# Performance work log

Measured on AMD Instinct MI355X. Metric: run time of the kernel, lower is better.

The kernel has to match this reference:

```python
import jax, jax.numpy as jnp
import numpy as np

B, N, D = 4, 2048, 512
H, DH = 8, 64
MLP = 2048
EPS = 1e-5


def setup_inputs() -> dict:
    key = jax.random.key(0)
    ks = jax.random.split(key, 8)
    s = lambda fan_in: 1.0 / np.sqrt(fan_in)
    return {
        "x": jax.random.normal(ks[0], (B, N, D), jnp.float32),
        "ln1_g": jnp.ones((D,), jnp.float32),
        "ln1_b": jnp.zeros((D,), jnp.float32),
        "Wqkv": jax.random.normal(ks[1], (D, 3 * H * DH), jnp.float32) * s(D),
        "temperature": jnp.asarray(np.log(DH ** -0.5), jnp.float32),
        "Wo": jax.random.normal(ks[2], (H * DH, D), jnp.float32) * s(H * DH),
        "bo": jnp.zeros((D,), jnp.float32),
        "ln2_g": jnp.ones((D,), jnp.float32),
        "ln2_b": jnp.zeros((D,), jnp.float32),
        "W1": jax.random.normal(ks[3], (D, MLP), jnp.float32) * s(D),
        "b1": jnp.zeros((MLP,), jnp.float32),
        "W2": jax.random.normal(ks[4], (MLP, D), jnp.float32) * s(MLP),
        "b2": jnp.zeros((D,), jnp.float32),
    }


def _layernorm(x, g, b):
    mu = jnp.mean(x, axis=-1, keepdims=True)
    var = jnp.var(x, axis=-1, keepdims=True)
    return (x - mu) * jax.lax.rsqrt(var + EPS) * g + b


def _lsa(x, Wqkv, temperature, Wo, bo):
    b, n, _ = x.shape
    qkv = x @ Wqkv  # [b, n, 3*H*DH]
    q, k, v = jnp.split(qkv, 3, axis=-1)
    rs = lambda t: t.reshape(b, n, H, DH).transpose(0, 2, 1, 3)  # b h n d
    q, k, v = rs(q), rs(k), rs(v)
    dots = jnp.einsum("bhnd,bhmd->bhnm", q, k) * jnp.exp(temperature)
    mask_value = -jnp.finfo(dots.dtype).max
    eye = jnp.eye(n, dtype=bool)
    dots = jnp.where(eye, mask_value, dots)  # mask diagonal (LSA)
    attn = jax.nn.softmax(dots, axis=-1)
    out = jnp.einsum("bhnm,bhmd->bhnd", attn, v)
    out = out.transpose(0, 2, 1, 3).reshape(b, n, H * DH)
    return out @ Wo + bo


def _ffn(x, W1, b1, W2, b2):
    h = jax.nn.gelu(x @ W1 + b1, approximate=False)
    return h @ W2 + b2


def reference(x, ln1_g, ln1_b, Wqkv, temperature, Wo, bo,
              ln2_g, ln2_b, W1, b1, W2, b2):
    y = _lsa(_layernorm(x, ln1_g, ln1_b), Wqkv, temperature, Wo, bo) + x
    z = _ffn(_layernorm(y, ln2_g, ln2_b), W1, b1, W2, b2) + y
    return (z, x)
```

## Files before the change

kernel.cpp:

```cpp
#include <hip/hip_runtime.h>
#include <math.h>

typedef __attribute__((ext_vector_type(4))) float f32x4;
typedef __attribute__((ext_vector_type(8))) short short8;

#define DEV __device__ __forceinline__

DEV short f2bf(float f){
  union { float f; unsigned u; } v; v.f = f;
  unsigned r = v.u + 0x7fffu + ((v.u >> 16) & 1u);
  return (short)(r >> 16);
}
DEV float bf2f(short s){
  union { unsigned u; float f; } v; v.u = ((unsigned)(unsigned short)s) << 16; return v.f;
}
DEV float exp2_hw(float x){ float r; asm("v_exp_f32 %0, %1" : "=v"(r) : "v"(x)); return r; }
DEV float rcp_hw(float x){ float r; asm("v_rcp_f32 %0, %1" : "=v"(r) : "v"(x)); return r; }
DEV unsigned cvtpk(float a, float b){
  unsigned r; asm("v_cvt_pk_bf16_f32 %0, %1, %2" : "=v"(r) : "v"(a), "v"(b)); return r;
}
DEV void gload_lds16(const short* src, short* lds){
  __builtin_amdgcn_global_load_lds(
      (const __attribute__((address_space(1))) void*)src,
      (__attribute__((address_space(3))) void*)lds, 16, 0, 0);
}
DEV float gelu_fast(float v){
  float u = v * (0.79788456f + 0.03567741f * v * v);
  float e = exp2_hw(u * 2.88539008f);
  float th = 1.0f - 2.0f * rcp_hw(e + 1.0f);
  return 0.5f * v * (1.0f + th);
}

__global__ __launch_bounds__(256) void transpose_bf16_kernel(
    const float* __restrict__ W, short* __restrict__ Wt, int K, int N)
{
  __shared__ float tile[32][33];
  int nb = blockIdx.x * 32, kb = blockIdx.y * 32;
  int tx = threadIdx.x & 31, ty = threadIdx.x >> 5;
  #pragma unroll
  for (int i = ty; i < 32; i += 8)
    tile[i][tx] = W[(size_t)(kb + i) * N + nb + tx];
  __syncthreads();
  #pragma unroll
  for (int i = ty; i < 32; i += 8)
    Wt[(size_t)(nb + i) * K + kb + tx] = f2bf(tile[tx][i]);
}

template<int COPYX>
__global__ __launch_bounds__(256) void ln_kernel(
    const float* __restrict__ x, const float* __restrict__ g,
    const float* __restrict__ b, short* __restrict__ out,
    float* __restrict__ xcopy)
{
  int row  = blockIdx.x * 4 + (threadIdx.x >> 6);
  int lane = threadIdx.x & 63;
  const float* xr = x + (size_t)row * 512 + lane * 8;
  f32x4 v0 = *(const f32x4*)(xr);
  f32x4 v1 = *(const f32x4*)(xr + 4);
  float s  = (v0[0]+v0[1]+v0[2]+v0[3]) + (v1[0]+v1[1]+v1[2]+v1[3]);
  float sq = (v0[0]*v0[0]+v0[1]*v0[1]+v0[2]*v0[2]+v0[3]*v0[3])
           + (v1[0]*v1[0]+v1[1]*v1[1]+v1[2]*v1[2]+v1[3]*v1[3]);
  #pragma unroll
  for (int off = 1; off < 64; off <<= 1) {
    s  += __shfl_xor(s, off);
    sq += __shfl_xor(sq, off);
  }
  float mu  = s * (1.0f / 512.0f);
  float var = sq * (1.0f / 512.0f) - mu * mu;
  float rstd = rsqrtf(var + 1e-5f);
  f32x4 g0 = *(const f32x4*)(g + lane * 8);
  f32x4 g1 = *(const f32x4*)(g + lane * 8 + 4);
  f32x4 b0 = *(const f32x4*)(b + lane * 8);
  f32x4 b1 = *(const f32x4*)(b + lane * 8 + 4);
  float o[8];
  #pragma unroll
  for (int j = 0; j < 4; ++j) o[j]     = (v0[j] - mu) * rstd * g0[j] + b0[j];
  #pragma unroll
  for (int j = 0; j < 4; ++j) o[4 + j] = (v1[j] - mu) * rstd * g1[j] + b1[j];
  uint4 pk;
  pk.x = cvtpk(o[0], o[1]); pk.y = cvtpk(o[2], o[3]);
  pk.z = cvtpk(o[4], o[5]); pk.w = cvtpk(o[6], o[7]);
  *(uint4*)(out + (size_t)row * 512 + lane * 8) = pk;
  if (COPYX) {
    float* xc = xcopy + (size_t)row * 512 + lane * 8;
    *(f32x4*)(xc)     = v0;
    *(f32x4*)(xc + 4) = v1;
  }
}

__global__ __launch_bounds__(256) void ln_bf_kernel(
    const short* __restrict__ x, const float* __restrict__ g,
    const float* __restrict__ b, short* __restrict__ out)
{
  int row  = blockIdx.x * 4 + (threadIdx.x >> 6);
  int lane = threadIdx.x & 63;
  short8 raw = *(const short8*)(x + (size_t)row * 512 + lane * 8);
  float v[8];
  #pragma unroll
  for (int j = 0; j < 8; ++j) v[j] = bf2f(raw[j]);
  float s = 0.f, sq = 0.f;
  #pragma unroll
  for (int j = 0; j < 8; ++j) { s += v[j]; sq += v[j] * v[j]; }
  #pragma unroll
  for (int off = 1; off < 64; off <<= 1) {
    s  += __shfl_xor(s, off);
    sq += __shfl_xor(sq, off);
  }
  float mu  = s * (1.0f / 512.0f);
  float var = sq * (1.0f / 512.0f) - mu * mu;
  float rstd = rsqrtf(var + 1e-5f);
  f32x4 g0 = *(const f32x4*)(g + lane * 8);
  f32x4 g1 = *(const f32x4*)(g + lane * 8 + 4);
  f32x4 b0 = *(const f32x4*)(b + lane * 8);
  f32x4 b1 = *(const f32x4*)(b + lane * 8 + 4);
  float o[8];
  #pragma unroll
  for (int j = 0; j < 4; ++j) o[j]     = (v[j] - mu) * rstd * g0[j] + b0[j];
  #pragma unroll
  for (int j = 0; j < 4; ++j) o[4 + j] = (v[4+j] - mu) * rstd * g1[j] + b1[j];
  uint4 pk;
  pk.x = cvtpk(o[0], o[1]); pk.y = cvtpk(o[2], o[3]);
  pk.z = cvtpk(o[4], o[5]); pk.w = cvtpk(o[6], o[7]);
  *(uint4*)(out + (size_t)row * 512 + lane * 8) = pk;
}

template<int EPI, int BM, typename OutT>
__global__ __launch_bounds__(256) void gemm_bt_kernel(
    const short* __restrict__ A, const short* __restrict__ Bt,
    OutT* __restrict__ C, const float* __restrict__ bias,
    const float* __restrict__ resid, const short* __restrict__ residb,
    int M, int N, int K)
{
  constexpr int MFR = BM / 32;
  constexpr int NFR = 4;
  constexpr int AI  = BM / 64;
  constexpr int BUF = BM * 32 + 128 * 32;
  __shared__ __align__(16) short smem[3 * BUF];

  int tid = threadIdx.x;
  int lane = tid & 63, wid = tid >> 6;
  int l16 = lane & 15, lq = lane >> 4;

  int gx = gridDim.x;
  int nwg = gx * gridDim.y;
  int orig = blockIdx.y * gx + blockIdx.x;
  int swz = (orig & 7) * (nwg >> 3) + (orig >> 3);
  int bn = swz % gx, bm = swz / gx;

  int wm = wid >> 1, wn = wid & 1;

  const short* gaP[AI];
  const short* gbP[2];
  #pragma unroll
  for (int i = 0; i < AI; ++i) {
    int gg = i * 4 + wid;
    gaP[i] = A + (size_t)(bm * BM + gg * 16 + l16) * K + lq * 8;
  }
  #pragma unroll
  for (int i = 0; i < 2; ++i) {
    int gg = i * 4 + wid;
    gbP[i] = Bt + (size_t)(bn * 128 + gg * 16 + l16) * K + lq * 8;
  }

  auto STAGE = [&](int bufi, int k0) {
    short* base = smem + bufi * BUF;
    #pragma unroll
    for (int i = 0; i < AI; ++i)
      gload_lds16(gaP[i] + k0, base + (i * 4 + wid) * 512);
    #pragma unroll
    for (int i = 0; i < 2; ++i)
      gload_lds16(gbP[i] + k0, base + BM * 32 + (i * 4 + wid) * 512);
  };

  f32x4 acc[MFR][NFR] = {};

  STAGE(0, 0);
  STAGE(1, 32);

  int nt = K >> 5;
  for (int t = 0; t < nt; ++t) {
    if (t + 1 < nt) {
      if constexpr (AI == 2) asm volatile("s_waitcnt vmcnt(4)" ::: "memory");
      else                   asm volatile("s_waitcnt vmcnt(3)" ::: "memory");
    } else {
      asm volatile("s_waitcnt vmcnt(0)" ::: "memory");
    }
    __builtin_amdgcn_s_barrier();
    __builtin_amdgcn_sched_barrier(0);
    if (t + 2 < nt) STAGE((t + 2) % 3, (t + 2) << 5);

    const short* base = smem + (t % 3) * BUF;
    short8 af[MFR], bfr[NFR];
    #pragma unroll
    for (int m = 0; m < MFR; ++m)
      af[m] = *(const short8*)(base + (wm * MFR + m) * 512 + lane * 8);
    #pragma unroll
    for (int n = 0; n < NFR; ++n)
      bfr[n] = *(const short8*)(base + BM * 32 + (wn * NFR + n) * 512 + lane * 8);
    __builtin_amdgcn_s_setprio(1);
    #pragma unroll
    for (int m = 0; m < MFR; ++m)
      #pragma unroll
      for (int n = 0; n < NFR; ++n)
        acc[m][n] = __builtin_amdgcn_mfma_f32_16x16x32_bf16(af[m], bfr[n], acc[m][n], 0, 0, 0);
    __builtin_amdgcn_s_setprio(0);
  }

  float bv[NFR];
  #pragma unroll
  for (int n = 0; n < NFR; ++n)
    bv[n] = bias[bn * 128 + (wn * NFR + n) * 16 + l16];

  #pragma unroll
  for (int m = 0; m < MFR; ++m) {
    #pragma unroll
    for (int r = 0; r < 4; ++r) {
      int row = bm * BM + (wm * MFR + m) * 16 + lq * 4 + r;
      #pragma unroll
      for (int n = 0; n < NFR; ++n) {
        int col = bn * 128 + (wn * NFR + n) * 16 + l16;
        float v = acc[m][n][r] + bv[n];
        if (EPI == 4) v += resid[(size_t)row * N + col];
        if (EPI == 5) v += bf2f(residb[(size_t)row * N + col]);
        if constexpr (sizeof(OutT) == 2)
          ((short*)C)[(size_t)row * N + col] = f2bf(v);
        else
          ((float*)C)[(size_t)row * N + col] = v;
      }
    }
  }
}

template<int EPI>
__global__ __launch_bounds__(512) void gemm256_kernel(
    const short* __restrict__ A, const short* __restrict__ Bt,
    short* __restrict__ C, const float* __restrict__ bias,
    short* __restrict__ vt, int M, int N, int K)
{
  constexpr int BUF = 24576;
  __shared__ __align__(16) short smem[3 * BUF];

  int tid = threadIdx.x;
  int lane = tid & 63, wid = tid >> 6;
  int l16 = lane & 15, lq = lane >> 4;

  int gx = gridDim.x;
  int nwg = gx * gridDim.y;
  int orig = blockIdx.y * gx + blockIdx.x;
  int swz = (orig & 7) * (nwg >> 3) + (orig >> 3);
  int bn = swz % gx, bm = swz / gx;

  int wm = wid >> 1, wn = wid & 1;

  const short* gaP[4];
  const short* gbP[2];
  #pragma unroll
  for (int i = 0; i < 4; ++i) {
    int g = i * 8 + wid;
    gaP[i] = A + (size_t)(bm * 256 + (g >> 1) * 16 + l16) * K + (g & 1) * 32 + lq * 8;
  }
  #pragma unroll
  for (int i = 0; i < 2; ++i) {
    int g = i * 8 + wid;
    gbP[i] = Bt + (size_t)(bn * 128 + (g >> 1) * 16 + l16) * K + (g & 1) * 32 + lq * 8;
  }

  auto STAGE = [&](int bufi, int k0) {
    short* base = smem + bufi * BUF;
    #pragma unroll
    for (int i = 0; i < 4; ++i)
      gload_lds16(gaP[i] + k0, base + (i * 8 + wid) * 512);
    #pragma unroll
    for (int i = 0; i < 2; ++i)
      gload_lds16(gbP[i] + k0, base + 16384 + (i * 8 + wid) * 512);
  };

  f32x4 acc[4][4] = {};

  STAGE(0, 0);
  STAGE(1, 64);

  int nt = K >> 6;
  for (int t = 0; t < nt; ++t) {
    if (t + 1 < nt) asm volatile("s_waitcnt vmcnt(6)" ::: "memory");
    else            asm volatile("s_waitcnt vmcnt(0)" ::: "memory");
    __builtin_amdgcn_s_barrier();
    __builtin_amdgcn_sched_barrier(0);
    if (t + 2 < nt) STAGE((t + 2) % 3, (t + 2) << 6);

    const short* base = smem + (t % 3) * BUF;
    #pragma unroll
    for (int kc = 0; kc < 2; ++kc) {
      short8 af[4], bfr[4];
      #pragma unroll
      for (int m = 0; m < 4; ++m)
        af[m] = *(const short8*)(base + ((wm * 4 + m) * 2 + kc) * 512 + lane * 8);
      #pragma unroll
      for (int n = 0; n < 4; ++n)
        bfr[n] = *(const short8*)(base + 16384 + ((wn * 4 + n) * 2 + kc) * 512 + lane * 8);
      __builtin_amdgcn_s_setprio(1);
      #pragma unroll
      for (int m = 0; m < 4; ++m)
        #pragma unroll
        for (int n = 0; n < 4; ++n)
          acc[m][n] = __builtin_amdgcn_mfma_f32_16x16x32_bf16(af[m], bfr[n], acc[m][n], 0, 0, 0);
      __builtin_amdgcn_s_setprio(0);
    }
  }

  if (EPI == 3 && bn >= 8) {
    __syncthreads();
    short* T = smem;
    #pragma unroll
    for (int m = 0; m < 4; ++m)
      #pragma unroll
      for (int n = 0; n < 4; ++n) {
        int c = wn * 64 + n * 16 + l16;
        #pragma unroll
        for (int r = 0; r < 4; ++r) {
          int rowl = wm * 64 + m * 16 + lq * 4 + r;
          T[c * 256 + (rowl ^ ((c & 7) << 4))] = f2bf(acc[m][n][r]);
        }
      }
    __syncthreads();
    int b2 = bm >> 3;
    int nnb = (bm & 7) * 256;
    int tn = tid & 31, cw = tid >> 5;
    #pragma unroll
    for (int c8 = 0; c8 < 8; ++c8) {
      int c = c8 * 16 + cw;
      short8 v = *(const short8*)(T + c * 256 + ((tn * 8) ^ ((c & 7) << 4)));
      if (tn & 1) {
        short8 w;
        #pragma unroll
        for (int j = 0; j < 8; ++j) w[j] = v[j ^ 4];
        v = w;
      }
      int c2 = bn * 128 + c - 1024;
      int bh = b2 * 8 + (c2 >> 6);
      int d  = c2 & 63;
      *(short8*)(vt + ((size_t)(bh * 64 + d)) * 2048 + nnb + tn * 8) = v;
    }
    return;
  }

  float bv[4];
  #pragma unroll
  for (int n = 0; n < 4; ++n)
    bv[n] = (EPI == 2) ? bias[bn * 128 + (wn * 4 + n) * 16 + l16] : 0.0f;

  #pragma unroll
  for (int m = 0; m < 4; ++m) {
    #pragma unroll
    for (int r = 0; r < 4; ++r) {
      int row = bm * 256 + (wm * 4 + m) * 16 + lq * 4 + r;
      #pragma unroll
      for (int n = 0; n < 4; ++n) {
        int col = bn * 128 + (wn * 4 + n) * 16 + l16;
        float v = acc[m][n][r];
        if (EPI == 2) v = gelu_fast(v + bv[n]);
        C[(size_t)row * N + col] = f2bf(v);
      }
    }
  }
}

__global__ __launch_bounds__(256, 2) void attn_kernel(
    const short* __restrict__ qkv, const short* __restrict__ vt,
    const float* __restrict__ temp_ptr,
    short* __restrict__ Op0, short* __restrict__ Op1, float* __restrict__ Lbuf)
{
  __shared__ __align__(16) short smem[16384];

  int tid = threadIdx.x;
  int lane = tid & 63, wid = tid >> 6;
  int l16 = lane & 15, lq = lane >> 4;
  int hi = lq >> 1, lq0 = lq & 1;

  int orig = blockIdx.y * 16 + blockIdx.x;
  int swz = (orig & 7) * 128 + (orig >> 3);
  int qb = swz & 15;
  int rr = swz >> 4;
  int bh = rr & 31, slice = rr >> 5;
  int b = bh >> 3, h = bh & 7;

  const short* qbase = qkv + (size_t)b * 2048 * 1536 + h * 64;
  const short* kbase = qbase + 512;
  const short* vbase = vt + (size_t)bh * 64 * 2048;
  int kslice = slice * 1024;

  float scale = __expf(temp_ptr[0]) * 1.44269504f;
  int q0 = qb * 128 + wid * 32;

  short8 qfrag[2][2];
  #pragma unroll
  for (int qf = 0; qf < 2; ++qf) {
    int qrow = q0 + qf * 16 + l16;
    #pragma unroll
    for (int c = 0; c < 2; ++c) {
      short8 raw = *(const short8*)(qbase + (size_t)qrow * 1536 + c * 32 + lq * 8);
      short8 sc;
      #pragma unroll
      for (int j = 0; j < 8; ++j) sc[j] = f2bf(bf2f(raw[j]) * scale);
      qfrag[qf][c] = sc;
    }
  }

  f32x4 accO[2][4] = {};
  float l[2] = {0.f, 0.f};

  auto STAGE = [&](int bufi, int k0) {
    #pragma unroll
    for (int i = 0; i < 2; ++i) {
      int w16 = i * 256 + tid;
      int sub = w16 >> 7;
      int cc  = (w16 >> 6) & 1;
      int lq2 = (w16 >> 4) & 3;
      int l2  = w16 & 15;
      const short* srcK = kbase + (size_t)(k0 + sub * 16 + l2) * 1536 + cc * 32 + lq2 * 8;
      gload_lds16(srcK, smem + bufi * 4096 + (i * 4 + wid) * 512);
      const short* srcV = vbase + (size_t)(sub * 16 + l2) * 2048 + k0 + cc * 32 + lq2 * 8;
      gload_lds16(srcV, smem + 8192 + bufi * 4096 + (i * 4 + wid) * 512);
    }
  };

  STAGE(0, kslice);
  asm volatile("s_waitcnt vmcnt(0)");
  __syncthreads();

  for (int t = 0; t < 16; ++t) {
    int cur = t & 1;
    int k0 = kslice + t * 64;
    if (t + 1 < 16) STAGE(cur ^ 1, k0 + 64);

    const short* kls = smem + cur * 4096;
    const short* vls = smem + 8192 + cur * 4096;

    f32x4 accS[2][4] = {};
    #pragma unroll
    for (int s = 0; s < 4; ++s) {
      short8 kf0 = *(const short8*)(kls + (s * 2 + 0) * 512 + lane * 8);
      short8 kf1 = *(const short8*)(kls + (s * 2 + 1) * 512 + lane * 8);
      #pragma unroll
      for (int qf = 0; qf < 2; ++qf) {
        accS[qf][s] = __builtin_amdgcn_mfma_f32_16x16x32_bf16(kf0, qfrag[qf][0], accS[qf][s], 0, 0, 0);
        accS[qf][s] = __builtin_amdgcn_mfma_f32_16x16x32_bf16(kf1, qfrag[qf][1], accS[qf][s], 0, 0, 0);
      }
    }

    if ((q0 & ~63) == k0) {
      #pragma unroll
      for (int qf = 0; qf < 2; ++qf) {
        int qg = q0 + qf * 16 + l16;
        #pragma unroll
        for (int s = 0; s < 4; ++s)
          #pragma unroll
          for (int r = 0; r < 4; ++r)
            if (k0 + s * 16 + lq * 4 + r == qg) accS[qf][s][r] = -30000.f;
      }
    }

    short8 pa[2][2];
    #pragma unroll
    for (int qf = 0; qf < 2; ++qf) {
      float sum = 0.f;
      unsigned W[4][2];
      #pragma unroll
      for (int s = 0; s < 4; ++s) {
        float p0 = exp2_hw(accS[qf][s][0]);
        float p1 = exp2_hw(accS[qf][s][1]);
        float p2 = exp2_hw(accS[qf][s][2]);
        float p3 = exp2_hw(accS[qf][s][3]);
        sum += (p0 + p1) + (p2 + p3);
        W[s][0] = cvtpk(p0, p1);
        W[s][1] = cvtpk(p2, p3);
      }
      sum += __shfl_xor(sum, 16);
      sum += __shfl_xor(sum, 32);
      l[qf] += sum;

      unsigned K0[2], S0[2], K2[2], S2[2], R0[2], R2[2];
      #pragma unroll
      for (int w = 0; w < 2; ++w) {
        K0[w] = hi ? W[1][w] : W[0][w];
        S0[w] = hi ? W[0][w] : W[1][w];
        K2[w] = hi ? W[3][w] : W[2][w];
        S2[w] = hi ? W[2][w] : W[3][w];
      }
      #pragma unroll
      for (int w = 0; w < 2; ++w) {
        R0[w] = (unsigned)__shfl_xor((int)S0[w], 32);
        R2[w] = (unsigned)__shfl_xor((int)S2[w], 32);
      }
      bool sw = (hi != lq0);
      unsigned FA[2], FB[2], sA[2], sB[2], GA[2], GB[2];
      #pragma unroll
      for (int w = 0; w < 2; ++w) {
        sA[w] = sw ? K0[w] : R0[w];  FA[w] = sw ? R0[w] : K0[w];
        sB[w] = sw ? K2[w] : R2[w];  FB[w] = sw ? R2[w] : K2[w];
      }
      #pragma unroll
      for (int w = 0; w < 2; ++w) {
        GA[w] = (unsigned)__shfl_xor((int)sA[w], 16);
        GB[w] = (unsigned)__shfl_xor((int)sB[w], 16);
      }
      union { unsigned u[4]; short8 s8; } p0u, p1u;
      p0u.u[0] = FA[0]; p0u.u[1] = FA[1]; p0u.u[2] = GA[0]; p0u.u[3] = GA[1];
      p1u.u[0] = FB[0]; p1u.u[1] = FB[1]; p1u.u[2] = GB[0]; p1u.u[3] = GB[1];
      pa[qf][0] = p0u.s8;
      pa[qf][1] = p1u.s8;
    }

    short8 vfr[4][2];
    #pragma unroll
    for (int d = 0; d < 4; ++d) {
      vfr[d][0] = *(const short8*)(vls + (d * 2 + 0) * 512 + lane * 8);
      vfr[d][1] = *(const short8*)(vls + (d * 2 + 1) * 512 + lane * 8);
    }
    #pragma unroll
    for (int qf = 0; qf < 2; ++qf)
      #pragma unroll
      for (int d = 0; d < 4; ++d) {
        accO[qf][d] = __builtin_amdgcn_mfma_f32_16x16x32_bf16(vfr[d][0], pa[qf][0], accO[qf][d], 0, 0, 0);
        accO[qf][d] = __builtin_amdgcn_mfma_f32_16x16x32_bf16(vfr[d][1], pa[qf][1], accO[qf][d], 0, 0, 0);
      }

    __syncthreads();
  }

  short* op = slice ? Op1 : Op0;
  #pragma unroll
  for (int qf = 0; qf < 2; ++qf) {
    int qg = q0 + qf * 16 + l16;
    if (lq == 0) Lbuf[(size_t)(slice * 32 + bh) * 2048 + qg] = l[qf];
    size_t rowoff = (size_t)(b * 2048 + qg) * 512 + h * 64;
    #pragma unroll
    for (int d = 0; d < 4; ++d) {
      unsigned w0 = cvtpk(accO[qf][d][0], accO[qf][d][1]);
      unsigned w1 = cvtpk(accO[qf][d][2], accO[qf][d][3]);
      uint2 pk; pk.x = w0; pk.y = w1;
      *(uint2*)(op + rowoff + d * 16 + lq * 4) = pk;
    }
  }
}

__global__ __launch_bounds__(256) void attn_combine_kernel(
    const short* __restrict__ Op0, const short* __restrict__ Op1,
    const float* __restrict__ Lbuf, short* __restrict__ out)
{
  int idx = blockIdx.x * 256 + threadIdx.x;
  size_t e = (size_t)idx * 8;
  int row = (int)(e >> 9);
  int col = (int)(e & 511);
  int b = row >> 11, q = row & 2047;
  int bh = b * 8 + (col >> 6);
  float l0 = Lbuf[(size_t)bh * 2048 + q];
  float l1 = Lbuf[(size_t)(32 + bh) * 2048 + q];
  float inv = rcp_hw(l0 + l1);
  short8 a = *(const short8*)(Op0 + e);
  short8 c = *(const short8*)(Op1 + e);
  float o[8];
  #pragma unroll
  for (int j = 0; j < 8; ++j) o[j] = (bf2f(a[j]) + bf2f(c[j])) * inv;
  uint4 pk;
  pk.x = cvtpk(o[0], o[1]); pk.y = cvtpk(o[2], o[3]);
  pk.z = cvtpk(o[4], o[5]); pk.w = cvtpk(o[6], o[7]);
  *(uint4*)(out + e) = pk;
}

extern "C" void kernel_launch(void* const* d_in, const int* in_sizes, int n_in,
                              void* d_out, int out_size, void* d_ws, size_t ws_size,
                              hipStream_t stream)
{
  const float* x    = (const float*)d_in[0];
  const float* ln1g = (const float*)d_in[1];
  const float* ln1b = (const float*)d_in[2];
  const float* Wqkv = (const float*)d_in[3];
  const float* temp = (const float*)d_in[4];
  const float* Wo   = (const float*)d_in[5];
  const float* bo   = (const float*)d_in[6];
  const float* ln2g = (const float*)d_in[7];
  const float* ln2b = (const float*)d_in[8];
  const float* W1   = (const float*)d_in[9];
  const float* b1   = (const float*)d_in[10];
  const float* W2   = (const float*)d_in[11];
  const float* b2   = (const float*)d_in[12];
  float* out = (float*)d_out;

  char* ws = (char*)d_ws;
  short* wqkv_t = (short*)(ws);
  float* lpart  = (float*)(ws);
  short* wo_t   = (short*)(ws + 1572864);
  short* w1_t   = (short*)(ws + 2097152);
  short* w2_t   = (short*)(ws + 4194304);
  short* h      = (short*)(ws + 6291456);
  short* qkv    = (short*)(ws + 14680064);
  short* attn   = (short*)(ws + 39845888);
  short* ybf    = (short*)(ws + 48234496);
  short* vt     = (short*)(ws + 48234496);
  short* t      = (short*)(ws + 14680064);

  const int M = 8192;

  transpose_bf16_kernel<<<dim3(1536 / 32, 512 / 32),  256, 0, stream>>>(Wqkv, wqkv_t, 512, 1536);
  transpose_bf16_kernel<<<dim3(512 / 32, 512 / 32),   256, 0, stream>>>(Wo,   wo_t,   512, 512);
  transpose_bf16_kernel<<<dim3(2048 / 32, 512 / 32),  256, 0, stream>>>(W1,   w1_t,   512, 2048);
  transpose_bf16_kernel<<<dim3(512 / 32, 2048 / 32),  256, 0, stream>>>(W2,   w2_t,   2048, 512);

  ln_kernel<1><<<M / 4, 256, 0, stream>>>(x, ln1g, ln1b, h, out + (size_t)M * 512);

  gemm256_kernel<3><<<dim3(1536 / 128, M / 256), 512, 0, stream>>>(
      h, wqkv_t, qkv, nullptr, vt, M, 1536, 512);

  attn_kernel<<<dim3(16, 64), 256, 0, stream>>>(qkv, vt, temp, attn, h, lpart);
  attn_combine_kernel<<<M * 512 / 8 / 256, 256, 0, stream>>>(attn, h, lpart, attn);

  gemm_bt_kernel<4, 64, short><<<dim3(512 / 128, M / 64), 256, 0, stream>>>(
      attn, wo_t, ybf, bo, x, nullptr, M, 512, 512);

  ln_bf_kernel<<<M / 4, 256, 0, stream>>>(ybf, ln2g, ln2b, h);

  gemm256_kernel<2><<<dim3(2048 / 128, M / 256), 512, 0, stream>>>(
      h, w1_t, t, b1, nullptr, M, 2048, 512);

  gemm_bt_kernel<5, 64, float><<<dim3(512 / 128, M / 64), 256, 0, stream>>>(
      t, w2_t, out, b2, nullptr, ybf, M, 512, 2048);
}
```

Measured before the change: 210.8 us.

## Halve attention query tile per block and merge weight transposes into one launch

The attention kernel now has each wave handle 16 query rows instead of 32, with 64 queries per block, which doubles the grid and drops the launch-bounds occupancy hint. Every K/V tile staged into LDS is therefore reused by half as many queries, doubling K/V global traffic in exchange for more blocks and lower register pressure. Separately, the four weight-transpose launches are folded into a single kernel that selects its matrix from the block index, removing three launch overheads.

Result: slower. 222.9 us (+5.7%).

```diff
diff --git a/kernel.cpp b/kernel.cpp
--- a/kernel.cpp
+++ b/kernel.cpp
@@ -31,11 +31,20 @@
   return 0.5f * v * (1.0f + th);
 }
 
-__global__ __launch_bounds__(256) void transpose_bf16_kernel(
-    const float* __restrict__ W, short* __restrict__ Wt, int K, int N)
-{
+__global__ __launch_bounds__(256) void transpose_all_kernel(
+    const float* __restrict__ Wqkv, short* __restrict__ wqkv_t,
+    const float* __restrict__ Wo,   short* __restrict__ wo_t,
+    const float* __restrict__ W1,   short* __restrict__ w1_t,
+    const float* __restrict__ W2,   short* __restrict__ w2_t)
+{
+  int bid = blockIdx.x;
+  const float* W; short* Wt; int K, N, nbx, local;
+  if (bid < 768)       { W = Wqkv; Wt = wqkv_t; K = 512;  N = 1536; nbx = 48; local = bid; }
+  else if (bid < 1024) { W = Wo;   Wt = wo_t;   K = 512;  N = 512;  nbx = 16; local = bid - 768; }
+  else if (bid < 2048) { W = W1;   Wt = w1_t;   K = 512;  N = 2048; nbx = 64; local = bid - 1024; }
+  else                 { W = W2;   Wt = w2_t;   K = 2048; N = 512;  nbx = 16; local = bid - 2048; }
   __shared__ float tile[32][33];
-  int nb = blockIdx.x * 32, kb = blockIdx.y * 32;
+  int nb = (local % nbx) * 32, kb = (local / nbx) * 32;
   int tx = threadIdx.x & 31, ty = threadIdx.x >> 5;
   #pragma unroll
   for (int i = ty; i < 32; i += 8)
@@ -365,7 +374,7 @@
   }
 }
 
-__global__ __launch_bounds__(256, 2) void attn_kernel(
+__global__ __launch_bounds__(256) void attn_kernel(
     const short* __restrict__ qkv, const short* __restrict__ vt,
     const float* __restrict__ temp_ptr,
     short* __restrict__ Op0, short* __restrict__ Op1, float* __restrict__ Lbuf)
@@ -377,10 +386,10 @@
   int l16 = lane & 15, lq = lane >> 4;
   int hi = lq >> 1, lq0 = lq & 1;
 
-  int orig = blockIdx.y * 16 + blockIdx.x;
-  int swz = (orig & 7) * 128 + (orig >> 3);
-  int qb = swz & 15;
-  int rr = swz >> 4;
+  int orig = blockIdx.y * 32 + blockIdx.x;
+  int swz = (orig & 7) * 256 + (orig >> 3);
+  int qb = swz & 31;
+  int rr = swz >> 5;
   int bh = rr & 31, slice = rr >> 5;
   int b = bh >> 3, h = bh & 7;
 
@@ -390,24 +399,23 @@
   int kslice = slice * 1024;
 
   float scale = __expf(temp_ptr[0]) * 1.44269504f;
-  int q0 = qb * 128 + wid * 32;
-
-  short8 qfrag[2][2];
-  #pragma unroll
-  for (int qf = 0; qf < 2; ++qf) {
-    int qrow = q0 + qf * 16 + l16;
+  int q0 = qb * 64 + wid * 16;
+
+  short8 qfrag[2];
+  {
+    int qrow = q0 + l16;
     #pragma unroll
     for (int c = 0; c < 2; ++c) {
       short8 raw = *(const short8*)(qbase + (size_t)qrow * 1536 + c * 32 + lq * 8);
       short8 sc;
       #pragma unroll
       for (int j = 0; j < 8; ++j) sc[j] = f2bf(bf2f(raw[j]) * scale);
-      qfrag[qf][c] = sc;
-    }
-  }
-
-  f32x4 accO[2][4] = {};
-  float l[2] = {0.f, 0.f};
+      qfrag[c] = sc;
+    }
+  }
+
+  f32x4 accO[4] = {};
+  float l = 0.f;
 
   auto STAGE = [&](int bufi, int k0) {
     #pragma unroll
@@ -436,48 +444,41 @@
     const short* kls = smem + cur * 4096;
     const short* vls = smem + 8192 + cur * 4096;
 
-    f32x4 accS[2][4] = {};
+    f32x4 accS[4] = {};
     #pragma unroll
     for (int s = 0; s < 4; ++s) {
       short8 kf0 = *(const short8*)(kls + (s * 2 + 0) * 512 + lane * 8);
       short8 kf1 = *(const short8*)(kls + (s * 2 + 1) * 512 + lane * 8);
-      #pragma unroll
-      for (int qf = 0; qf < 2; ++qf) {
-        accS[qf][s] = __builtin_amdgcn_mfma_f32_16x16x32_bf16(kf0, qfrag[qf][0], accS[qf][s], 0, 0, 0);
-        accS[qf][s] = __builtin_amdgcn_mfma_f32_16x16x32_bf16(kf1, qfrag[qf][1], accS[qf][s], 0, 0, 0);
-      }
-    }
-
-    if ((q0 & ~63) == k0) {
-      #pragma unroll
-      for (int qf = 0; qf < 2; ++qf) {
-        int qg = q0 + qf * 16 + l16;
+      accS[s] = __builtin_amdgcn_mfma_f32_16x16x32_bf16(kf0, qfrag[0], accS[s], 0, 0, 0);
+      accS[s] = __builtin_amdgcn_mfma_f32_16x16x32_bf16(kf1, qfrag[1], accS[s], 0, 0, 0);
+    }
+
+    if (qb * 64 == k0) {
+      int qg = q0 + l16;
+      #pragma unroll
+      for (int s = 0; s < 4; ++s)
         #pragma unroll
-        for (int s = 0; s < 4; ++s)
-          #pragma unroll
-          for (int r = 0; r < 4; ++r)
-            if (k0 + s * 16 + lq * 4 + r == qg) accS[qf][s][r] = -30000.f;
-      }
-    }
-
-    short8 pa[2][2];
-    #pragma unroll
-    for (int qf = 0; qf < 2; ++qf) {
+        for (int r = 0; r < 4; ++r)
+          if (k0 + s * 16 + lq * 4 + r == qg) accS[s][r] = -30000.f;
+    }
+
+    short8 pa[2];
+    {
       float sum = 0.f;
       unsigned W[4][2];
       #pragma unroll
       for (int s = 0; s < 4; ++s) {
-        float p0 = exp2_hw(accS[qf][s][0]);
-        float p1 = exp2_hw(accS[qf][s][1]);
-        float p2 = exp2_hw(accS[qf][s][2]);
-        float p3 = exp2_hw(accS[qf][s][3]);
+        float p0 = exp2_hw(accS[s][0]);
+        float p1 = exp2_hw(accS[s][1]);
+        float p2 = exp2_hw(accS[s][2]);
+        float p3 = exp2_hw(accS[s][3]);
         sum += (p0 + p1) + (p2 + p3);
         W[s][0] = cvtpk(p0, p1);
         W[s][1] = cvtpk(p2, p3);
       }
       sum += __shfl_xor(sum, 16);
       sum += __shfl_xor(sum, 32);
-      l[qf] += sum;
+      l += sum;
 
       unsigned K0[2], S0[2], K2[2], S2[2], R0[2], R2[2];
       #pragma unroll
@@ -507,40 +508,31 @@
       union { unsigned u[4]; short8 s8; } p0u, p1u;
       p0u.u[0] = FA[0]; p0u.u[1] = FA[1]; p0u.u[2] = GA[0]; p0u.u[3] = GA[1];
       p1u.u[0] = FB[0]; p1u.u[1] = FB[1]; p1u.u[2] = GB[0]; p1u.u[3] = GB[1];
-      pa[qf][0] = p0u.s8;
-      pa[qf][1] = p1u.s8;
-    }
-
-    short8 vfr[4][2];
+      pa[0] = p0u.s8;
+      pa[1] = p1u.s8;
+    }
+
     #pragma unroll
     for (int d = 0; d < 4; ++d) {
-      vfr[d][0] = *(const short8*)(vls + (d * 2 + 0) * 512 + lane * 8);
-      vfr[d][1] = *(const short8*)(vls + (d * 2 + 1) * 512 + lane * 8);
-    }
-    #pragma unroll
-    for (int qf = 0; qf < 2; ++qf)
-      #pragma unroll
-      for (int d = 0; d < 4; ++d) {
-        accO[qf][d] = __builtin_amdgcn_mfma_f32_16x16x32_bf16(vfr[d][0], pa[qf][0], accO[qf][d], 0, 0, 0);
-        accO[qf][d] = __builtin_amdgcn_mfma_f32_16x16x32_bf16(vfr[d][1], pa[qf][1], accO[qf][d], 0, 0, 0);
-      }
+      short8 vf0 = *(const short8*)(vls + (d * 2 + 0) * 512 + lane * 8);
+      short8 vf1 = *(const short8*)(vls + (d * 2 + 1) * 512 + lane * 8);
+      accO[d] = __builtin_amdgcn_mfma_f32_16x16x32_bf16(vf0, pa[0], accO[d], 0, 0, 0);
+      accO[d] = __builtin_amdgcn_mfma_f32_16x16x32_bf16(vf1, pa[1], accO[d], 0, 0, 0);
+    }
 
     __syncthreads();
   }
 
   short* op = slice ? Op1 : Op0;
-  #pragma unroll
-  for (int qf = 0; qf < 2; ++qf) {
-    int qg = q0 + qf * 16 + l16;
-    if (lq == 0) Lbuf[(size_t)(slice * 32 + bh) * 2048 + qg] = l[qf];
-    size_t rowoff = (size_t)(b * 2048 + qg) * 512 + h * 64;
-    #pragma unroll
-    for (int d = 0; d < 4; ++d) {
-      unsigned w0 = cvtpk(accO[qf][d][0], accO[qf][d][1]);
-      unsigned w1 = cvtpk(accO[qf][d][2], accO[qf][d][3]);
-      uint2 pk; pk.x = w0; pk.y = w1;
-      *(uint2*)(op + rowoff + d * 16 + lq * 4) = pk;
-    }
+  int qg = q0 + l16;
+  if (lq == 0) Lbuf[(size_t)(slice * 32 + bh) * 2048 + qg] = l;
+  size_t rowoff = (size_t)(b * 2048 + qg) * 512 + h * 64;
+  #pragma unroll
+  for (int d = 0; d < 4; ++d) {
+    unsigned w0 = cvtpk(accO[d][0], accO[d][1]);
+    unsigned w1 = cvtpk(accO[d][2], accO[d][3]);
+    uint2 pk; pk.x = w0; pk.y = w1;
+    *(uint2*)(op + rowoff + d * 16 + lq * 4) = pk;
   }
 }
 
@@ -602,17 +594,15 @@
 
   const int M = 8192;
 
-  transpose_bf16_kernel<<<dim3(1536 / 32, 512 / 32),  256, 0, stream>>>(Wqkv, wqkv_t, 512, 1536);
-  transpose_bf16_kernel<<<dim3(512 / 32, 512 / 32),   256, 0, stream>>>(Wo,   wo_t,   512, 512);
-  transpose_bf16_kernel<<<dim3(2048 / 32, 512 / 32),  256, 0, stream>>>(W1,   w1_t,   512, 2048);
-  transpose_bf16_kernel<<<dim3(512 / 32, 2048 / 32),  256, 0, stream>>>(W2,   w2_t,   2048, 512);
+  transpose_all_kernel<<<3072, 256, 0, stream>>>(
+      Wqkv, wqkv_t, Wo, wo_t, W1, w1_t, W2, w2_t);
 
   ln_kernel<1><<<M / 4, 256, 0, stream>>>(x, ln1g, ln1b, h, out + (size_t)M * 512);
 
   gemm256_kernel<3><<<dim3(1536 / 128, M / 256), 512, 0, stream>>>(
       h, wqkv_t, qkv, nullptr, vt, M, 1536, 512);
 
-  attn_kernel<<<dim3(16, 64), 256, 0, stream>>>(qkv, vt, temp, attn, h, lpart);
+  attn_kernel<<<dim3(32, 64), 256, 0, stream>>>(qkv, vt, temp, attn, h, lpart);
   attn_combine_kernel<<<M * 512 / 8 / 256, 256, 0, stream>>>(attn, h, lpart, attn);
 
   gemm_bt_kernel<4, 64, short><<<dim3(512 / 128, M / 64), 256, 0, stream>>>(
```
